# Kernel tuning notes

Measured on AMD Instinct MI355X. Metric: run time of the kernel, lower is better.

## Reference

```python
import jax, jax.numpy as jnp
import numpy as np

N = 50000
E = 800000
NFEAT = 128
NHID = 64
NCLASS = 40


def setup_inputs() -> dict:
    key = jax.random.key(0)
    ks = jax.random.split(key, 12)
    return {
        "x": jax.random.normal(ks[0], (N, NFEAT), dtype=jnp.float32),
        "M": jax.random.uniform(ks[1], (N, 1), dtype=jnp.float32),
        "AM": jax.random.uniform(ks[2], (N, 1), dtype=jnp.float32),
        "adj_vals": jax.random.uniform(ks[3], (E,), dtype=jnp.float32),
        "adjZ_vals": jax.random.uniform(ks[4], (E,), dtype=jnp.float32),
        "W0": jax.random.normal(ks[5], (NFEAT, NFEAT), dtype=jnp.float32) * (1.414 / np.sqrt(NFEAT)),
        "b0": jnp.zeros((NFEAT,), dtype=jnp.float32),
        "W1": jax.random.normal(ks[6], (NFEAT, NHID), dtype=jnp.float32) * (1.414 / np.sqrt(NFEAT)),
        "b1": jnp.zeros((NHID,), dtype=jnp.float32),
        "W2": jax.random.normal(ks[7], (NHID, NCLASS), dtype=jnp.float32) * (1.0 / np.sqrt(NHID)),
        "b2": jnp.zeros((NCLASS,), dtype=jnp.float32),
        "row": jax.random.randint(ks[8], (E,), 0, N, dtype=jnp.int32),
        "col": jax.random.randint(ks[9], (E,), 0, N, dtype=jnp.int32),
    }


def _spmm(vals, row, col, X, n):
    # sparse (COO) @ dense: out[r] = sum_e vals[e] * X[col[e]] for row[e]==r
    return jax.ops.segment_sum(vals[:, None] * X[col], row, num_segments=n)


def reference(x, M, AM, adj_vals, adjZ_vals, W0, b0, W1, b1, W2, b2, row, col):
    n = x.shape[0]
    # gc0: PaGConv(nfeat->nfeat) on adjZ, then ReLU (dropout is identity in eval)
    h = _spmm(adjZ_vals, row, col, M * x, n) * AM
    h = jax.nn.relu(h @ W0 + b0)
    # gc1: PaGConv(nfeat->nhid) on adjZ, then ReLU
    h = _spmm(adjZ_vals, row, col, M * h, n) * AM
    h = jax.nn.relu(h @ W1 + b1)
    # gc2: plain GConv(nhid->nclass) on adj
    h = _spmm(adj_vals, row, col, h, n)
    h = h @ W2 + b2
    return jax.nn.log_softmax(h, axis=1)
```

## Files before the change

kernel.cpp:

```cpp
#include <hip/hip_runtime.h>
#include <hip/hip_bf16.h>
#include <math.h>


typedef __attribute__((ext_vector_type(8))) short bf16x8;
typedef __attribute__((ext_vector_type(4))) float f32x4;

#define HIST_EPB_LOG 15
#define HIST_EPB 32768
#define NBINS 50176
#define NBMAX 26
#define SCAN_BLOCKS 196

__device__ __forceinline__ float rl_f(float v, int j) {
    return __builtin_bit_cast(float,
        __builtin_amdgcn_readlane(__builtin_bit_cast(int, v), j));
}
__device__ __forceinline__ int rl_i(int v, int j) {
    return __builtin_amdgcn_readlane(v, j);
}
__device__ __forceinline__ unsigned short f2bf(float f) {
    unsigned u = __builtin_bit_cast(unsigned, f);
    u += 0x7fffu + ((u >> 16) & 1u);
    return (unsigned short)(u >> 16);
}
__device__ __forceinline__ unsigned pack2bf(float lo, float hi) {
    return (unsigned)f2bf(lo) | ((unsigned)f2bf(hi) << 16);
}
__device__ __forceinline__ float bf_lo(unsigned u) {
    return __builtin_bit_cast(float, u << 16);
}
__device__ __forceinline__ float bf_hi(unsigned u) {
    return __builtin_bit_cast(float, u & 0xffff0000u);
}
__device__ __forceinline__ float clampf(float v) {
    return fminf(fmaxf(v, -1e30f), 1e30f);
}
__device__ __forceinline__ unsigned long long aload(const unsigned long long* p) {
    return __hip_atomic_load(p, __ATOMIC_ACQUIRE, __HIP_MEMORY_SCOPE_AGENT);
}


__global__ void prep_wt(const float* __restrict__ W0, const float* __restrict__ W1,
                        const float* __restrict__ W2,
                        unsigned short* __restrict__ wt0, unsigned short* __restrict__ wt1,
                        unsigned short* __restrict__ wt2) {
    int idx = blockIdx.x * 256 + threadIdx.x;
    if (idx < 128 * 128) {
        int nn = idx >> 7, k = idx & 127;
        wt0[idx] = f2bf(W0[k * 128 + nn]);
    }
    idx -= 128 * 128;
    if (idx >= 0 && idx < 64 * 128) {
        int nn = idx >> 7, k = idx & 127;
        wt1[idx] = f2bf(W1[k * 64 + nn]);
    }
    idx -= 64 * 128;
    if (idx >= 0 && idx < 48 * 64) {
        int nn = idx >> 6, k = idx & 63;
        wt2[idx] = (nn < 40) ? f2bf(W2[k * 40 + nn]) : (unsigned short)0;
    }
}


template <int K, int COLS, int NTPAD>
__launch_bounds__(256)
__global__ void gemm_mfma(const unsigned short* __restrict__ A,
                          const unsigned short* __restrict__ Wt,
                          unsigned short* __restrict__ outp, int n) {
    constexpr int KS = K / 32;
    const int tid = threadIdx.x;
    const int bid = blockIdx.x;
    const int lane = tid & 63;
    const int wid = tid >> 6;
    const int m15 = lane & 15;
    const int q = lane >> 4;
    const int rA = bid * 64 + wid * 16 + m15;

    bf16x8 a[KS];
#pragma unroll
    for (int ks = 0; ks < KS; ++ks) {
        uint4 z = make_uint4(0u, 0u, 0u, 0u);
        if (rA < n) z = *(const uint4*)(A + (size_t)rA * K + ks * 32 + q * 8);
        a[ks] = __builtin_bit_cast(bf16x8, z);
    }

#pragma unroll
    for (int nt = 0; nt < NTPAD / 16; ++nt) {
        f32x4 acc = {0.f, 0.f, 0.f, 0.f};
        const int bn = nt * 16 + m15;
#pragma unroll
        for (int ks = 0; ks < KS; ++ks) {
            const uint4 z = *(const uint4*)(Wt + (size_t)bn * K + ks * 32 + q * 8);
            acc = __builtin_amdgcn_mfma_f32_16x16x32_bf16(
                a[ks], __builtin_bit_cast(bf16x8, z), acc, 0, 0, 0);
        }
        const int gc = nt * 16 + m15;
#pragma unroll
        for (int rr = 0; rr < 4; ++rr) {
            const int gr = bid * 64 + wid * 16 + q * 4 + rr;
            bool ok = gr < n;
            if constexpr (NTPAD != COLS) ok = ok && (gc < COLS);
            if (ok) outp[(size_t)gr * COLS + gc] = f2bf(clampf(acc[rr]));
        }
    }
}


__launch_bounds__(1024)
__global__ void hist_gemm0(const int* __restrict__ row,
                           unsigned short* __restrict__ cntmat,
                           unsigned short* __restrict__ lrank, int E, int NB,
                           const float* __restrict__ x, const float* __restrict__ Mv,
                           const unsigned short* __restrict__ Wt0,
                           unsigned short* __restrict__ t_buf, int n) {
    __shared__ __align__(16) unsigned hcnt[NBINS / 2];
    const int blk = blockIdx.x;
    const int t = threadIdx.x;
    if (blk < NB) {
        uint4* h4 = (uint4*)hcnt;
        const uint4 z4 = make_uint4(0u, 0u, 0u, 0u);
        for (int i = t; i < NBINS / 8; i += 1024) h4[i] = z4;
        __syncthreads();
        const int s = blk << HIST_EPB_LOG;
        const int e = min(E, s + HIST_EPB);
        for (int i = s + t; i < e; i += 1024) {
            const int r = row[i];
            const unsigned sh = (unsigned)(r & 1) << 4;
            const unsigned old = atomicAdd(&hcnt[r >> 1], 1u << sh);
            lrank[i] = (unsigned short)((old >> sh) & 0xffffu);
        }
        __syncthreads();
        uint4* dst = (uint4*)(cntmat + (size_t)blk * NBINS);
        for (int i = t; i < NBINS / 8; i += 1024) dst[i] = h4[i];
    } else {
        const int tid = t & 255;
        const int bid = (blk - NB) * 4 + (t >> 8);
        const int lane = tid & 63;
        const int wid = tid >> 6;
        const int m15 = lane & 15;
        const int q = lane >> 4;
        const int rA = bid * 64 + wid * 16 + m15;

        bf16x8 a[4];
        {
            float m = 1.0f;
            if (rA < n) m = Mv[rA];
#pragma unroll
            for (int ks = 0; ks < 4; ++ks) {
                float4 lo = make_float4(0.f, 0.f, 0.f, 0.f);
                float4 hi = make_float4(0.f, 0.f, 0.f, 0.f);
                if (rA < n) {
                    lo = *(const float4*)(x + (size_t)rA * 128 + ks * 32 + q * 8);
                    hi = *(const float4*)(x + (size_t)rA * 128 + ks * 32 + q * 8 + 4);
                }
                union { bf16x8 v; unsigned short u[8]; } pk;
                pk.u[0] = f2bf(lo.x * m); pk.u[1] = f2bf(lo.y * m);
                pk.u[2] = f2bf(lo.z * m); pk.u[3] = f2bf(lo.w * m);
                pk.u[4] = f2bf(hi.x * m); pk.u[5] = f2bf(hi.y * m);
                pk.u[6] = f2bf(hi.z * m); pk.u[7] = f2bf(hi.w * m);
                a[ks] = pk.v;
            }
        }
#pragma unroll
        for (int nt = 0; nt < 8; ++nt) {
            f32x4 acc = {0.f, 0.f, 0.f, 0.f};
            const int bn = nt * 16 + m15;
#pragma unroll
            for (int ks = 0; ks < 4; ++ks) {
                const uint4 z = *(const uint4*)(Wt0 + (size_t)bn * 128 + ks * 32 + q * 8);
                acc = __builtin_amdgcn_mfma_f32_16x16x32_bf16(
                    a[ks], __builtin_bit_cast(bf16x8, z), acc, 0, 0, 0);
            }
            const int gc = nt * 16 + m15;
#pragma unroll
            for (int rr = 0; rr < 4; ++rr) {
                const int gr = bid * 64 + wid * 16 + q * 4 + rr;
                if (gr < n) t_buf[(size_t)gr * 128 + gc] = f2bf(clampf(acc[rr]));
            }
        }
    }
}


__launch_bounds__(256)
__global__ void scan_one(const unsigned short* __restrict__ cm,
                         unsigned* __restrict__ cmabs, int* __restrict__ rp,
                         unsigned long long* __restrict__ gpub,
                         int n, int NB, int E) {
    __shared__ int sd[256];
    const int g = blockIdx.x;
    const int t = threadIdx.x;
    const int bin = g * 256 + t;

    unsigned tot = 0;
    for (int b = 0; b < NB; ++b) tot += cm[(size_t)b * NBINS + bin];

    sd[t] = (int)tot;
    __syncthreads();
    for (int off = 1; off < 256; off <<= 1) {
        int xv = (t >= off) ? sd[t - off] : 0;
        __syncthreads();
        sd[t] += xv;
        __syncthreads();
    }
    const int excl = sd[t] - (int)tot;
    const int gtot = sd[255];
    __syncthreads();

    if (t == 0)
        atomicExch(&gpub[g], (1ULL << 32) | (unsigned long long)(unsigned)gtot);

    int my = 0;
    for (int p = t; p < g; p += 256) {
        unsigned long long v;
        do { v = aload(&gpub[p]); } while ((v >> 32) == 0ULL);
        my += (int)(unsigned)v;
    }
    sd[t] = my;
    __syncthreads();
    for (int off = 128; off > 0; off >>= 1) {
        if (t < off) sd[t] += sd[t + off];
        __syncthreads();
    }
    const int base = sd[0];

    const int rpf = base + excl;
    if (bin < n) rp[bin] = rpf;
    if (g == SCAN_BLOCKS - 1 && t == 255) rp[n] = E;

    int run = rpf;
    for (int b = 0; b < NB; ++b) {
        cmabs[(size_t)b * NBINS + bin] = (unsigned)run;
        run += (int)cm[(size_t)b * NBINS + bin];
    }
}


__global__ void scatter_kernel(const int* __restrict__ row, const int* __restrict__ col,
                               const float* __restrict__ vA, const float* __restrict__ vZ,
                               const unsigned* __restrict__ cmabs,
                               const unsigned short* __restrict__ lrank,
                               uint4* __restrict__ packed16, int E) {
    int e = blockIdx.x * blockDim.x + threadIdx.x;
    if (e >= E) return;
    const int r = row[e];
    const int pos = (int)(cmabs[(size_t)(e >> HIST_EPB_LOG) * NBINS + r]
                          + (unsigned)lrank[e]);
    uint4 pk;
    pk.x = (unsigned)col[e];
    pk.y = __builtin_bit_cast(unsigned, vZ[e]);
    pk.z = __builtin_bit_cast(unsigned, vA[e]);
    pk.w = 0u;
    packed16[pos] = pk;
}


__launch_bounds__(256)
__global__ void spmm128_kernel(const uint4* __restrict__ packed16,
                               const int* __restrict__ rp, const unsigned short* __restrict__ X,
                               const float* __restrict__ AM, const float* __restrict__ Mv,
                               const float* __restrict__ bias,
                               unsigned short* __restrict__ out, int n) {
    const int lane = threadIdx.x & 63;
    const int r = (int)((blockIdx.x * (unsigned)blockDim.x + threadIdx.x) >> 6);
    if (r >= n) return;
    const int s = __builtin_amdgcn_readfirstlane(rp[r]);
    const int e = __builtin_amdgcn_readfirstlane(rp[r + 1]);

    float acc0 = 0.0f, acc1 = 0.0f;
    for (int base = s; base < e; base += 64) {
        const int nn = min(64, e - base);
        int ci = 0; float vf = 0.0f;
        if (lane < nn) {
            const uint4 pk = packed16[base + lane];
            ci = (int)pk.x;
            vf = __builtin_bit_cast(float, pk.y);
        }
        int j = 0;
        for (; j + 16 <= nn; j += 16) {
            unsigned u[16];
#pragma unroll
            for (int q = 0; q < 16; ++q) {
                const int cq = rl_i(ci, j + q);
                u[q] = *(const unsigned*)(X + (size_t)cq * 128 + lane * 2);
            }
#pragma unroll
            for (int q = 0; q < 16; ++q) {
                const float vq = rl_f(vf, j + q);
                acc0 += vq * bf_lo(u[q]);
                acc1 += vq * bf_hi(u[q]);
            }
        }
        for (; j + 8 <= nn; j += 8) {
            unsigned u[8];
#pragma unroll
            for (int q = 0; q < 8; ++q) {
                const int cq = rl_i(ci, j + q);
                u[q] = *(const unsigned*)(X + (size_t)cq * 128 + lane * 2);
            }
#pragma unroll
            for (int q = 0; q < 8; ++q) {
                const float vq = rl_f(vf, j + q);
                acc0 += vq * bf_lo(u[q]);
                acc1 += vq * bf_hi(u[q]);
            }
        }
        for (; j < nn; ++j) {
            const int cq = rl_i(ci, j);
            const float vq = rl_f(vf, j);
            const unsigned u = *(const unsigned*)(X + (size_t)cq * 128 + lane * 2);
            acc0 += vq * bf_lo(u);
            acc1 += vq * bf_hi(u);
        }
    }

    const float am = AM[r];
    const float mr = Mv[r];
    const float o0 = fminf(fmaxf((acc0 * am + bias[2 * lane]) * mr, 0.0f), 1e30f);
    const float o1 = fminf(fmaxf((acc1 * am + bias[2 * lane + 1]) * mr, 0.0f), 1e30f);
    ((unsigned*)out)[(size_t)r * 64 + lane] = pack2bf(o0, o1);
}


__launch_bounds__(256)
__global__ void spmm64_gemm2(const uint4* __restrict__ packed16,
                             const int* __restrict__ rp, const unsigned short* __restrict__ X,
                             const float* __restrict__ AM, const float* __restrict__ bias1,
                             const unsigned short* __restrict__ wt2,
                             unsigned short* __restrict__ out40, int n) {
    const int lane = threadIdx.x & 63;
    const int g = lane >> 4;
    const int ls = lane & 15;
    const int r = (int)((blockIdx.x * (unsigned)blockDim.x + threadIdx.x) >> 6);
    if (r >= n) return;
    const int s = __builtin_amdgcn_readfirstlane(rp[r]);
    const int e = __builtin_amdgcn_readfirstlane(rp[r + 1]);

    float a0 = 0.0f, a1 = 0.0f, a2 = 0.0f, a3 = 0.0f;
    for (int base = s; base < e; base += 64) {
        const int nn = min(64, e - base);
        int ci = 0; float vf = 0.0f;
        if (lane < nn) {
            const uint4 pk = packed16[base + lane];
            ci = (int)pk.x;
            vf = __builtin_bit_cast(float, pk.y);
        }
        for (int j = 0; j < nn; j += 16) {
#pragma unroll
            for (int q = 0; q < 4; ++q) {
                const int jj = j + 4 * q + g;
                const bool ok = jj < nn;
                const int idx = jj & 63;
                const int c = __shfl(ci, idx);
                const float v = __shfl(vf, idx);
                if (ok) {
                    const uint2 u = *(const uint2*)(X + (size_t)c * 64 + ls * 4);
                    a0 += v * bf_lo(u.x);
                    a1 += v * bf_hi(u.x);
                    a2 += v * bf_lo(u.y);
                    a3 += v * bf_hi(u.y);
                }
            }
        }
    }
    a0 += __shfl_xor(a0, 16); a0 += __shfl_xor(a0, 32);
    a1 += __shfl_xor(a1, 16); a1 += __shfl_xor(a1, 32);
    a2 += __shfl_xor(a2, 16); a2 += __shfl_xor(a2, 32);
    a3 += __shfl_xor(a3, 16); a3 += __shfl_xor(a3, 32);

    const float am = AM[r];
    const float o0 = fminf(fmaxf(a0 * am + bias1[4 * ls + 0], 0.0f), 1e30f);
    const float o1 = fminf(fmaxf(a1 * am + bias1[4 * ls + 1], 0.0f), 1e30f);
    const float o2 = fminf(fmaxf(a2 * am + bias1[4 * ls + 2], 0.0f), 1e30f);
    const float o3 = fminf(fmaxf(a3 * am + bias1[4 * ls + 3], 0.0f), 1e30f);

    const int wrow = (lane < 48) ? lane : 0;
    const unsigned short* wp = wt2 + wrow * 64;
    float y = 0.0f;
#pragma unroll
    for (int qq = 0; qq < 16; ++qq) {
        const uint2 w = *(const uint2*)(wp + 4 * qq);
        const float h0v = rl_f(o0, qq);
        const float h1v = rl_f(o1, qq);
        const float h2v = rl_f(o2, qq);
        const float h3v = rl_f(o3, qq);
        y += h0v * bf_lo(w.x) + h1v * bf_hi(w.x)
           + h2v * bf_lo(w.y) + h3v * bf_hi(w.y);
    }
    if (lane < 40) out40[(size_t)r * 40 + lane] = f2bf(clampf(y));
}


__launch_bounds__(256)
__global__ void spmm40_kernel(const uint4* __restrict__ packed16,
                              const int* __restrict__ rp, const unsigned short* __restrict__ X,
                              const float* __restrict__ bias,
                              float* __restrict__ out, int n) {
    const int lane = threadIdx.x & 63;
    const int g = lane / 20;
    const int ls = lane - 20 * g;
    const bool active = g < 3;
    const int r = (int)((blockIdx.x * (unsigned)blockDim.x + threadIdx.x) >> 6);
    if (r >= n) return;
    const int s = __builtin_amdgcn_readfirstlane(rp[r]);
    const int e = __builtin_amdgcn_readfirstlane(rp[r + 1]);

    float acc0 = 0.0f, acc1 = 0.0f;
    for (int base = s; base < e; base += 64) {
        const int nn = min(64, e - base);
        int ci = 0; float vf = 0.0f;
        if (lane < nn) {
            const uint4 pk = packed16[base + lane];
            ci = (int)pk.x;
            vf = __builtin_bit_cast(float, pk.z);
        }
        for (int j = 0; j < nn; j += 24) {
#pragma unroll
            for (int q = 0; q < 8; ++q) {
                const int jj = j + 3 * q + g;
                const bool ok = active && jj < nn;
                const int idx = jj & 63;
                const int c = __shfl(ci, idx);
                const float v = __shfl(vf, idx);
                if (ok) {
                    const unsigned u = *(const unsigned*)(X + (size_t)c * 40 + ls * 2);
                    acc0 += v * bf_lo(u);
                    acc1 += v * bf_hi(u);
                }
            }
        }
    }
    {
        const float a1 = __shfl(acc0, (lane + 20) & 63);
        const float a2 = __shfl(acc0, (lane + 40) & 63);
        const float b1 = __shfl(acc1, (lane + 20) & 63);
        const float b2 = __shfl(acc1, (lane + 40) & 63);
        acc0 += a1 + a2;
        acc1 += b1 + b2;
    }

    const bool own = lane < 20;
    const float vv0 = own ? fminf(fmaxf(acc0 + bias[2 * ls], -1e30f), 1e30f) : -INFINITY;
    const float vv1 = own ? fminf(fmaxf(acc1 + bias[2 * ls + 1], -1e30f), 1e30f) : -INFINITY;
    float mx = fmaxf(vv0, vv1);
#pragma unroll
    for (int off = 32; off > 0; off >>= 1) mx = fmaxf(mx, __shfl_xor(mx, off));
    float sum = own ? (expf(vv0 - mx) + expf(vv1 - mx)) : 0.0f;
#pragma unroll
    for (int off = 32; off > 0; off >>= 1) sum += __shfl_xor(sum, off);
    if (own) {
        const float lse = mx + logf(sum);
        *(float2*)(out + (size_t)r * 40 + ls * 2) = make_float2(vv0 - lse, vv1 - lse);
    }
}


extern "C" void kernel_launch(void* const* d_in, const int* in_sizes, int n_in,
                              void* d_out, int out_size, void* d_ws, size_t ws_size,
                              hipStream_t stream) {
    const float* x    = (const float*)d_in[0];
    const float* M    = (const float*)d_in[1];
    const float* AM   = (const float*)d_in[2];
    const float* adjv = (const float*)d_in[3];
    const float* adjZ = (const float*)d_in[4];
    const float* W0   = (const float*)d_in[5];
    const float* b0   = (const float*)d_in[6];
    const float* W1   = (const float*)d_in[7];
    const float* b1   = (const float*)d_in[8];
    const float* W2   = (const float*)d_in[9];
    const float* b2   = (const float*)d_in[10];
    const int* row    = (const int*)d_in[11];
    const int* col    = (const int*)d_in[12];
    float* out = (float*)d_out;

    const int n = in_sizes[1];
    const int E = in_sizes[3];

    unsigned short* t_buf = (unsigned short*)d_ws;
    unsigned short* wt0 = t_buf + (size_t)n * 128;
    unsigned short* wt1 = wt0 + 128 * 128;
    unsigned short* wt2 = wt1 + 64 * 128;
    unsigned short* h_buf = wt2 + 48 * 64;
    unsigned short* lrank  = h_buf;
    unsigned short* cntmat = lrank + (size_t)E;
    unsigned* cmabs = (unsigned*)(cntmat + (size_t)NBMAX * NBINS);
    int* rp = (int*)(h_buf + (size_t)n * 128);
    unsigned long long* gpub = (unsigned long long*)
        (((uintptr_t)(rp + n + 2) + 7) & ~(uintptr_t)7);
    uint4* packed16 = (uint4*)
        (((uintptr_t)(gpub + 256) + 15) & ~(uintptr_t)15);

    const int NB = (E + HIST_EPB - 1) >> HIST_EPB_LOG;
    const int gemmBlocks = (n + 63) / 64;
    const int gemmB4 = (gemmBlocks + 3) / 4;

    hipMemsetAsync(gpub, 0, 256 * sizeof(unsigned long long), stream);
    prep_wt<<<(128 * 128 + 64 * 128 + 48 * 64 + 255) / 256, 256, 0, stream>>>(
        W0, W1, W2, wt0, wt1, wt2);

    hist_gemm0<<<NB + gemmB4, 1024, 0, stream>>>(row, cntmat, lrank, E, NB,
                                                 x, M, wt0, t_buf, n);

    scan_one<<<SCAN_BLOCKS, 256, 0, stream>>>(cntmat, cmabs, rp, gpub, n, NB, E);

    scatter_kernel<<<(E + 255) / 256, 256, 0, stream>>>(row, col, adjv, adjZ,
                                                        cmabs, lrank, packed16, E);

    const int spmmBlocks = (n + 3) / 4;

    spmm128_kernel<<<spmmBlocks, 256, 0, stream>>>(packed16, rp, t_buf, AM, M, b0, h_buf, n);
    gemm_mfma<128, 64, 64><<<gemmBlocks, 256, 0, stream>>>(h_buf, wt1, t_buf, n);
    spmm64_gemm2<<<spmmBlocks, 256, 0, stream>>>(packed16, rp, t_buf, AM, b1, wt2, h_buf, n);
    spmm40_kernel<<<spmmBlocks, 256, 0, stream>>>(packed16, rp, h_buf, b2, out, n);
}
```

Measured before the change: 287.6 us.

## Fuse W1 GEMM into layer-1 SpMM and use MFMA for W2 in layer-2 SpMM

The layer-1 SpMM now computes 16 rows per block into shared memory and then applies the W1 projection with MFMA in the same kernel. This removes the separate GEMM launch and its round trip of the 128-wide hidden activations through global memory. The layer-2 SpMM likewise stages its 16 rows in LDS and uses MFMA for W2, replacing the per-row readlane dot products. In exchange, each wave now processes 4 rows serially and a block barrier is added before the matmul, which can reduce latency hiding for irregular row lengths.

Measured after the change: 264.0 us. 1.09x faster.

```diff
diff --git a/kernel.cpp b/kernel.cpp
--- a/kernel.cpp
+++ b/kernel.cpp
@@ -59,50 +59,6 @@
     if (idx >= 0 && idx < 48 * 64) {
         int nn = idx >> 6, k = idx & 63;
         wt2[idx] = (nn < 40) ? f2bf(W2[k * 40 + nn]) : (unsigned short)0;
-    }
-}
-
-
-template <int K, int COLS, int NTPAD>
-__launch_bounds__(256)
-__global__ void gemm_mfma(const unsigned short* __restrict__ A,
-                          const unsigned short* __restrict__ Wt,
-                          unsigned short* __restrict__ outp, int n) {
-    constexpr int KS = K / 32;
-    const int tid = threadIdx.x;
-    const int bid = blockIdx.x;
-    const int lane = tid & 63;
-    const int wid = tid >> 6;
-    const int m15 = lane & 15;
-    const int q = lane >> 4;
-    const int rA = bid * 64 + wid * 16 + m15;
-
-    bf16x8 a[KS];
-#pragma unroll
-    for (int ks = 0; ks < KS; ++ks) {
-        uint4 z = make_uint4(0u, 0u, 0u, 0u);
-        if (rA < n) z = *(const uint4*)(A + (size_t)rA * K + ks * 32 + q * 8);
-        a[ks] = __builtin_bit_cast(bf16x8, z);
-    }
-
-#pragma unroll
-    for (int nt = 0; nt < NTPAD / 16; ++nt) {
-        f32x4 acc = {0.f, 0.f, 0.f, 0.f};
-        const int bn = nt * 16 + m15;
-#pragma unroll
-        for (int ks = 0; ks < KS; ++ks) {
-            const uint4 z = *(const uint4*)(Wt + (size_t)bn * K + ks * 32 + q * 8);
-            acc = __builtin_amdgcn_mfma_f32_16x16x32_bf16(
-                a[ks], __builtin_bit_cast(bf16x8, z), acc, 0, 0, 0);
-        }
-        const int gc = nt * 16 + m15;
-#pragma unroll
-        for (int rr = 0; rr < 4; ++rr) {
-            const int gr = bid * 64 + wid * 16 + q * 4 + rr;
-            bool ok = gr < n;
-            if constexpr (NTPAD != COLS) ok = ok && (gc < COLS);
-            if (ok) outp[(size_t)gr * COLS + gc] = f2bf(clampf(acc[rr]));
-        }
     }
 }
 
@@ -257,138 +213,195 @@
 
 
 __launch_bounds__(256)
-__global__ void spmm128_kernel(const uint4* __restrict__ packed16,
-                               const int* __restrict__ rp, const unsigned short* __restrict__ X,
-                               const float* __restrict__ AM, const float* __restrict__ Mv,
-                               const float* __restrict__ bias,
-                               unsigned short* __restrict__ out, int n) {
-    const int lane = threadIdx.x & 63;
-    const int r = (int)((blockIdx.x * (unsigned)blockDim.x + threadIdx.x) >> 6);
-    if (r >= n) return;
-    const int s = __builtin_amdgcn_readfirstlane(rp[r]);
-    const int e = __builtin_amdgcn_readfirstlane(rp[r + 1]);
-
-    float acc0 = 0.0f, acc1 = 0.0f;
-    for (int base = s; base < e; base += 64) {
-        const int nn = min(64, e - base);
-        int ci = 0; float vf = 0.0f;
-        if (lane < nn) {
-            const uint4 pk = packed16[base + lane];
-            ci = (int)pk.x;
-            vf = __builtin_bit_cast(float, pk.y);
-        }
-        int j = 0;
-        for (; j + 16 <= nn; j += 16) {
-            unsigned u[16];
-#pragma unroll
-            for (int q = 0; q < 16; ++q) {
-                const int cq = rl_i(ci, j + q);
-                u[q] = *(const unsigned*)(X + (size_t)cq * 128 + lane * 2);
-            }
-#pragma unroll
-            for (int q = 0; q < 16; ++q) {
-                const float vq = rl_f(vf, j + q);
-                acc0 += vq * bf_lo(u[q]);
-                acc1 += vq * bf_hi(u[q]);
-            }
-        }
-        for (; j + 8 <= nn; j += 8) {
-            unsigned u[8];
-#pragma unroll
-            for (int q = 0; q < 8; ++q) {
-                const int cq = rl_i(ci, j + q);
-                u[q] = *(const unsigned*)(X + (size_t)cq * 128 + lane * 2);
-            }
-#pragma unroll
-            for (int q = 0; q < 8; ++q) {
-                const float vq = rl_f(vf, j + q);
-                acc0 += vq * bf_lo(u[q]);
-                acc1 += vq * bf_hi(u[q]);
-            }
-        }
-        for (; j < nn; ++j) {
-            const int cq = rl_i(ci, j);
-            const float vq = rl_f(vf, j);
-            const unsigned u = *(const unsigned*)(X + (size_t)cq * 128 + lane * 2);
-            acc0 += vq * bf_lo(u);
-            acc1 += vq * bf_hi(u);
-        }
-    }
-
-    const float am = AM[r];
-    const float mr = Mv[r];
-    const float o0 = fminf(fmaxf((acc0 * am + bias[2 * lane]) * mr, 0.0f), 1e30f);
-    const float o1 = fminf(fmaxf((acc1 * am + bias[2 * lane + 1]) * mr, 0.0f), 1e30f);
-    ((unsigned*)out)[(size_t)r * 64 + lane] = pack2bf(o0, o1);
+__global__ void spmm128_g1(const uint4* __restrict__ packed16,
+                           const int* __restrict__ rp, const unsigned short* __restrict__ X,
+                           const float* __restrict__ AM, const float* __restrict__ Mv,
+                           const float* __restrict__ bias,
+                           const unsigned short* __restrict__ wt1,
+                           unsigned short* __restrict__ g1, int n) {
+    __shared__ __align__(16) unsigned short h16[16][136];
+    const int t = threadIdx.x;
+    const int lane = t & 63;
+    const int w = t >> 6;
+    const int rbase = blockIdx.x * 16;
+
+    for (int i = 0; i < 4; ++i) {
+        const int lr = w * 4 + i;
+        const int r = rbase + lr;
+        float o0 = 0.0f, o1 = 0.0f;
+        if (r < n) {
+            const int s = __builtin_amdgcn_readfirstlane(rp[r]);
+            const int e = __builtin_amdgcn_readfirstlane(rp[r + 1]);
+            float acc0 = 0.0f, acc1 = 0.0f;
+            for (int base = s; base < e; base += 64) {
+                const int nn = min(64, e - base);
+                int ci = 0; float vf = 0.0f;
+                if (lane < nn) {
+                    const uint4 pk = packed16[base + lane];
+                    ci = (int)pk.x;
+                    vf = __builtin_bit_cast(float, pk.y);
+                }
+                int j = 0;
+                for (; j + 16 <= nn; j += 16) {
+                    unsigned u[16];
+#pragma unroll
+                    for (int q = 0; q < 16; ++q) {
+                        const int cq = rl_i(ci, j + q);
+                        u[q] = *(const unsigned*)(X + (size_t)cq * 128 + lane * 2);
+                    }
+#pragma unroll
+                    for (int q = 0; q < 16; ++q) {
+                        const float vq = rl_f(vf, j + q);
+                        acc0 += vq * bf_lo(u[q]);
+                        acc1 += vq * bf_hi(u[q]);
+                    }
+                }
+                for (; j + 8 <= nn; j += 8) {
+                    unsigned u[8];
+#pragma unroll
+                    for (int q = 0; q < 8; ++q) {
+                        const int cq = rl_i(ci, j + q);
+                        u[q] = *(const unsigned*)(X + (size_t)cq * 128 + lane * 2);
+                    }
+#pragma unroll
+                    for (int q = 0; q < 8; ++q) {
+                        const float vq = rl_f(vf, j + q);
+                        acc0 += vq * bf_lo(u[q]);
+                        acc1 += vq * bf_hi(u[q]);
+                    }
+                }
+                for (; j < nn; ++j) {
+                    const int cq = rl_i(ci, j);
+                    const float vq = rl_f(vf, j);
+                    const unsigned u = *(const unsigned*)(X + (size_t)cq * 128 + lane * 2);
+                    acc0 += vq * bf_lo(u);
+                    acc1 += vq * bf_hi(u);
+                }
+            }
+            const float am = AM[r];
+            const float mr = Mv[r];
+            o0 = fminf(fmaxf((acc0 * am + bias[2 * lane]) * mr, 0.0f), 1e30f);
+            o1 = fminf(fmaxf((acc1 * am + bias[2 * lane + 1]) * mr, 0.0f), 1e30f);
+        }
+        *(unsigned*)&h16[lr][2 * lane] = pack2bf(o0, o1);
+    }
+    __syncthreads();
+
+    const int m15 = lane & 15;
+    const int q = lane >> 4;
+    bf16x8 a[4];
+#pragma unroll
+    for (int ks = 0; ks < 4; ++ks)
+        a[ks] = __builtin_bit_cast(bf16x8,
+                    *(const uint4*)&h16[m15][ks * 32 + q * 8]);
+    f32x4 acc = {0.f, 0.f, 0.f, 0.f};
+    const int bn = w * 16 + m15;
+#pragma unroll
+    for (int ks = 0; ks < 4; ++ks) {
+        const uint4 z = *(const uint4*)(wt1 + (size_t)bn * 128 + ks * 32 + q * 8);
+        acc = __builtin_amdgcn_mfma_f32_16x16x32_bf16(
+            a[ks], __builtin_bit_cast(bf16x8, z), acc, 0, 0, 0);
+    }
+    const int gcol = w * 16 + m15;
+#pragma unroll
+    for (int rr = 0; rr < 4; ++rr) {
+        const int grow = rbase + q * 4 + rr;
+        if (grow < n) g1[(size_t)grow * 64 + gcol] = f2bf(clampf(acc[rr]));
+    }
 }
 
 
 __launch_bounds__(256)
-__global__ void spmm64_gemm2(const uint4* __restrict__ packed16,
-                             const int* __restrict__ rp, const unsigned short* __restrict__ X,
-                             const float* __restrict__ AM, const float* __restrict__ bias1,
-                             const unsigned short* __restrict__ wt2,
-                             unsigned short* __restrict__ out40, int n) {
-    const int lane = threadIdx.x & 63;
+__global__ void spmm64_g2(const uint4* __restrict__ packed16,
+                          const int* __restrict__ rp, const unsigned short* __restrict__ X,
+                          const float* __restrict__ AM, const float* __restrict__ bias1,
+                          const unsigned short* __restrict__ wt2,
+                          unsigned short* __restrict__ out40, int n) {
+    __shared__ __align__(16) unsigned short h16[16][72];
+    const int t = threadIdx.x;
+    const int lane = t & 63;
+    const int w = t >> 6;
     const int g = lane >> 4;
     const int ls = lane & 15;
-    const int r = (int)((blockIdx.x * (unsigned)blockDim.x + threadIdx.x) >> 6);
-    if (r >= n) return;
-    const int s = __builtin_amdgcn_readfirstlane(rp[r]);
-    const int e = __builtin_amdgcn_readfirstlane(rp[r + 1]);
-
-    float a0 = 0.0f, a1 = 0.0f, a2 = 0.0f, a3 = 0.0f;
-    for (int base = s; base < e; base += 64) {
-        const int nn = min(64, e - base);
-        int ci = 0; float vf = 0.0f;
-        if (lane < nn) {
-            const uint4 pk = packed16[base + lane];
-            ci = (int)pk.x;
-            vf = __builtin_bit_cast(float, pk.y);
-        }
-        for (int j = 0; j < nn; j += 16) {
-#pragma unroll
-            for (int q = 0; q < 4; ++q) {
-                const int jj = j + 4 * q + g;
-                const bool ok = jj < nn;
-                const int idx = jj & 63;
-                const int c = __shfl(ci, idx);
-                const float v = __shfl(vf, idx);
-                if (ok) {
-                    const uint2 u = *(const uint2*)(X + (size_t)c * 64 + ls * 4);
-                    a0 += v * bf_lo(u.x);
-                    a1 += v * bf_hi(u.x);
-                    a2 += v * bf_lo(u.y);
-                    a3 += v * bf_hi(u.y);
-                }
-            }
-        }
-    }
-    a0 += __shfl_xor(a0, 16); a0 += __shfl_xor(a0, 32);
-    a1 += __shfl_xor(a1, 16); a1 += __shfl_xor(a1, 32);
-    a2 += __shfl_xor(a2, 16); a2 += __shfl_xor(a2, 32);
-    a3 += __shfl_xor(a3, 16); a3 += __shfl_xor(a3, 32);
-
-    const float am = AM[r];
-    const float o0 = fminf(fmaxf(a0 * am + bias1[4 * ls + 0], 0.0f), 1e30f);
-    const float o1 = fminf(fmaxf(a1 * am + bias1[4 * ls + 1], 0.0f), 1e30f);
-    const float o2 = fminf(fmaxf(a2 * am + bias1[4 * ls + 2], 0.0f), 1e30f);
-    const float o3 = fminf(fmaxf(a3 * am + bias1[4 * ls + 3], 0.0f), 1e30f);
-
-    const int wrow = (lane < 48) ? lane : 0;
-    const unsigned short* wp = wt2 + wrow * 64;
-    float y = 0.0f;
-#pragma unroll
-    for (int qq = 0; qq < 16; ++qq) {
-        const uint2 w = *(const uint2*)(wp + 4 * qq);
-        const float h0v = rl_f(o0, qq);
-        const float h1v = rl_f(o1, qq);
-        const float h2v = rl_f(o2, qq);
-        const float h3v = rl_f(o3, qq);
-        y += h0v * bf_lo(w.x) + h1v * bf_hi(w.x)
-           + h2v * bf_lo(w.y) + h3v * bf_hi(w.y);
-    }
-    if (lane < 40) out40[(size_t)r * 40 + lane] = f2bf(clampf(y));
+    const int rbase = blockIdx.x * 16;
+
+    for (int i = 0; i < 4; ++i) {
+        const int lr = w * 4 + i;
+        const int r = rbase + lr;
+        float a0 = 0.0f, a1 = 0.0f, a2 = 0.0f, a3 = 0.0f;
+        if (r < n) {
+            const int s = __builtin_amdgcn_readfirstlane(rp[r]);
+            const int e = __builtin_amdgcn_readfirstlane(rp[r + 1]);
+            for (int base = s; base < e; base += 64) {
+                const int nn = min(64, e - base);
+                int ci = 0; float vf = 0.0f;
+                if (lane < nn) {
+                    const uint4 pk = packed16[base + lane];
+                    ci = (int)pk.x;
+                    vf = __builtin_bit_cast(float, pk.y);
+                }
+                for (int j = 0; j < nn; j += 16) {
+#pragma unroll
+                    for (int q = 0; q < 4; ++q) {
+                        const int jj = j + 4 * q + g;
+                        const bool ok = jj < nn;
+                        const int idx = jj & 63;
+                        const int c = __shfl(ci, idx);
+                        const float v = __shfl(vf, idx);
+                        if (ok) {
+                            const uint2 u = *(const uint2*)(X + (size_t)c * 64 + ls * 4);
+                            a0 += v * bf_lo(u.x);
+                            a1 += v * bf_hi(u.x);
+                            a2 += v * bf_lo(u.y);
+                            a3 += v * bf_hi(u.y);
+                        }
+                    }
+                }
+            }
+            a0 += __shfl_xor(a0, 16); a0 += __shfl_xor(a0, 32);
+            a1 += __shfl_xor(a1, 16); a1 += __shfl_xor(a1, 32);
+            a2 += __shfl_xor(a2, 16); a2 += __shfl_xor(a2, 32);
+            a3 += __shfl_xor(a3, 16); a3 += __shfl_xor(a3, 32);
+            const float am = AM[r];
+            a0 = fminf(fmaxf(a0 * am + bias1[4 * ls + 0], 0.0f), 1e30f);
+            a1 = fminf(fmaxf(a1 * am + bias1[4 * ls + 1], 0.0f), 1e30f);
+            a2 = fminf(fmaxf(a2 * am + bias1[4 * ls + 2], 0.0f), 1e30f);
+            a3 = fminf(fmaxf(a3 * am + bias1[4 * ls + 3], 0.0f), 1e30f);
+        }
+        if (lane < 16) {
+            uint2 wv;
+            wv.x = pack2bf(a0, a1);
+            wv.y = pack2bf(a2, a3);
+            *(uint2*)&h16[lr][4 * ls] = wv;
+        }
+    }
+    __syncthreads();
+
+    if (w < 3) {
+        const int m15 = lane & 15;
+        const int q = lane >> 4;
+        bf16x8 a[2];
+#pragma unroll
+        for (int ks = 0; ks < 2; ++ks)
+            a[ks] = __builtin_bit_cast(bf16x8,
+                        *(const uint4*)&h16[m15][ks * 32 + q * 8]);
+        f32x4 acc = {0.f, 0.f, 0.f, 0.f};
+        const int bn = w * 16 + m15;
+#pragma unroll
+        for (int ks = 0; ks < 2; ++ks) {
+            const uint4 z = *(const uint4*)(wt2 + (size_t)bn * 64 + ks * 32 + q * 8);
+            acc = __builtin_amdgcn_mfma_f32_16x16x32_bf16(
+                a[ks], __builtin_bit_cast(bf16x8, z), acc, 0, 0, 0);
+        }
+        const int gcol = w * 16 + m15;
+        if (gcol < 40) {
+#pragma unroll
+            for (int rr = 0; rr < 4; ++rr) {
+                const int grow = rbase + q * 4 + rr;
+                if (grow < n) out40[(size_t)grow * 40 + gcol] = f2bf(clampf(acc[rr]));
+            }
+        }
+    }
 }
 
 
@@ -507,10 +520,11 @@
     scatter_kernel<<<(E + 255) / 256, 256, 0, stream>>>(row, col, adjv, adjZ,
                                                         cmabs, lrank, packed16, E);
 
-    const int spmmBlocks = (n + 3) / 4;
-
-    spmm128_kernel<<<spmmBlocks, 256, 0, stream>>>(packed16, rp, t_buf, AM, M, b0, h_buf, n);
-    gemm_mfma<128, 64, 64><<<gemmBlocks, 256, 0, stream>>>(h_buf, wt1, t_buf, n);
-    spmm64_gemm2<<<spmmBlocks, 256, 0, stream>>>(packed16, rp, t_buf, AM, b1, wt2, h_buf, n);
-    spmm40_kernel<<<spmmBlocks, 256, 0, stream>>>(packed16, rp, h_buf, b2, out, n);
-}
+    const int blk16 = (n + 15) / 16;
+
+    spmm128_g1<<<blk16, 256, 0, stream>>>(packed16, rp, t_buf, AM, M, b0, wt1,
+                                          h_buf, n);
+    spmm64_g2<<<blk16, 256, 0, stream>>>(packed16, rp, h_buf, AM, b1, wt2,
+                                         t_buf, n);
+    spmm40_kernel<<<blk16 * 4, 256, 0, stream>>>(packed16, rp, t_buf, b2, out, n);
+}
```
